# Kernel optimization log

Measured on AMD Instinct MI355X. Metric: run time of the kernel, lower is better.

## Reference

```python
import jax, jax.numpy as jnp
import numpy as np

B, S, D, H = 2, 2048, 1024, 16
HD = D // H  # head dim = 64


def setup_inputs() -> dict:
    key = jax.random.key(0)
    ks = jax.random.split(key, 8)
    s = 0.02
    return {
        "Q": jax.random.normal(ks[0], (B, S, D), jnp.float32),
        "K": jax.random.normal(ks[1], (B, S, D), jnp.float32),
        "V": jax.random.normal(ks[2], (B, S, D), jnp.float32),
        "mask": jax.random.randint(ks[3], (1, 1, S, S), 0, 2, jnp.int32),
        "Wq": jax.random.normal(ks[4], (D, D), jnp.float32) * s,
        "bq": jnp.zeros((D,), jnp.float32),
        "Wk": jax.random.normal(ks[5], (D, D), jnp.float32) * s,
        "bk": jnp.zeros((D,), jnp.float32),
        "Wv": jax.random.normal(ks[6], (D, D), jnp.float32) * s,
        "bv": jnp.zeros((D,), jnp.float32),
        "Wo": jax.random.normal(ks[7], (D, D), jnp.float32) * s,
        "bo": jnp.zeros((D,), jnp.float32),
    }


def reference(Q, K, V, mask, Wq, bq, Wk, bk, Wv, bv, Wo, bo):
    b = Q.shape[0]
    # QKV projections, split into heads: [B,S,D] -> [B,H,S,HD]
    q = (Q @ Wq + bq).reshape(b, -1, H, HD).transpose(0, 2, 1, 3)
    k = (K @ Wk + bk).reshape(b, -1, H, HD).transpose(0, 2, 1, 3)
    v = (V @ Wv + bv).reshape(b, -1, H, HD).transpose(0, 2, 1, 3)
    # scaled dot-product attention with full [B,H,S,S] scores (as in source)
    scale = jnp.sqrt(jnp.asarray(HD, q.dtype))
    scores = jnp.einsum("bhqd,bhkd->bhqk", q, k) / scale
    scores = jnp.where(mask == 0, -jnp.inf, scores)
    attn = jax.nn.softmax(scores, axis=-1)
    ctx = jnp.einsum("bhqk,bhkd->bhqd", attn, v)
    # merge heads and output projection
    concat = ctx.transpose(0, 2, 1, 3).reshape(b, -1, H * HD)
    return concat @ Wo + bo
```

## Files before the change

### kernel.cpp

```cpp
#include <hip/hip_runtime.h>


using s8v = __attribute__((ext_vector_type(8))) short;
using f4v = __attribute__((ext_vector_type(4))) float;
typedef unsigned long long u64;

__device__ __forceinline__ unsigned short f2bf(float f) {
  union { float f; unsigned int u; } v; v.f = f;
  return (unsigned short)((v.u + 0x7fffu + ((v.u >> 16) & 1u)) >> 16);
}

__global__ void f2b3_kernel(const float* __restrict__ A, const float* __restrict__ B,
                            const float* __restrict__ C, unsigned short* __restrict__ oA,
                            unsigned short* __restrict__ oB, unsigned short* __restrict__ oC) {
  int z = blockIdx.x >> 12;
  int idx = (blockIdx.x & 4095) * 256 + threadIdx.x;
  const float* in = (z == 0) ? A : (z == 1) ? B : C;
  unsigned short* out = (z == 0) ? oA : (z == 1) ? oB : oC;
  float4 v = ((const float4*)in)[idx];
  ushort4 o;
  o.x = f2bf(v.x); o.y = f2bf(v.y); o.z = f2bf(v.z); o.w = f2bf(v.w);
  ((ushort4*)out)[idx] = o;
}

__global__ void packmask_kernel(const int* __restrict__ mask, u64* __restrict__ bm) {
  int gw = (int)((blockIdx.x * 256 + threadIdx.x) >> 6);
  int lane = threadIdx.x & 63;
  int mv = mask[(size_t)gw * 64 + lane];
  u64 bal = __ballot(mv != 0);
  if (lane == 0) bm[gw] = bal;
}

__global__ void wtrans4_kernel(const float* __restrict__ W0, const float* __restrict__ W1,
                               const float* __restrict__ W2, const float* __restrict__ W3,
                               unsigned short* __restrict__ T0, unsigned short* __restrict__ T1,
                               unsigned short* __restrict__ T2, unsigned short* __restrict__ T3) {
  __shared__ unsigned short t[64][72];
  int z = blockIdx.z;
  const float* W = (z == 0) ? W0 : (z == 1) ? W1 : (z == 2) ? W2 : W3;
  unsigned short* Wt = (z == 0) ? T0 : (z == 1) ? T1 : (z == 2) ? T2 : T3;
  int k0 = blockIdx.x * 64, n0 = blockIdx.y * 64;
  int tid = threadIdx.x;
  for (int p = 0; p < 4; ++p) {
    int idx = p * 256 + tid;
    int row = idx >> 4;
    int c4  = idx & 15;
    float4 v = *(const float4*)&W[(size_t)(k0 + row) * 1024 + n0 + c4 * 4];
    t[row][c4 * 4 + 0] = f2bf(v.x);
    t[row][c4 * 4 + 1] = f2bf(v.y);
    t[row][c4 * 4 + 2] = f2bf(v.z);
    t[row][c4 * 4 + 3] = f2bf(v.w);
  }
  __syncthreads();
  for (int p = 0; p < 2; ++p) {
    int idx = p * 256 + tid;
    int j  = idx >> 3;
    int c8 = idx & 7;
    unsigned short tmp[8];
    for (int i = 0; i < 8; ++i) tmp[i] = t[c8 * 8 + i][j];
    uint4 o;
    o.x = tmp[0] | ((unsigned)tmp[1] << 16);
    o.y = tmp[2] | ((unsigned)tmp[3] << 16);
    o.z = tmp[4] | ((unsigned)tmp[5] << 16);
    o.w = tmp[6] | ((unsigned)tmp[7] << 16);
    *(uint4*)&Wt[(size_t)(n0 + j) * 1024 + k0 + c8 * 8] = o;
  }
}

__global__ __launch_bounds__(256) void proj3_kernel(
    const unsigned short* __restrict__ A0, const unsigned short* __restrict__ A1,
    const unsigned short* __restrict__ A2,
    const unsigned short* __restrict__ W0, const unsigned short* __restrict__ W1,
    const unsigned short* __restrict__ W2,
    const float* __restrict__ b0, const float* __restrict__ b1, const float* __restrict__ b2,
    unsigned short* __restrict__ oq, unsigned short* __restrict__ ok,
    unsigned short* __restrict__ ovt) {
  const int z = blockIdx.z;
  const unsigned short* A  = (z == 0) ? A0 : (z == 1) ? A1 : A2;
  const unsigned short* Wt = (z == 0) ? W0 : (z == 1) ? W1 : W2;
  const float* bias        = (z == 0) ? b0 : (z == 1) ? b1 : b2;

  __shared__ __align__(16) unsigned short As[128][40];
  __shared__ __align__(16) unsigned short Bs[128][40];

  const int tid = threadIdx.x;
  const int lane = tid & 63, w = tid >> 6, ln = lane & 15, quad = lane >> 4;
  const int wm = (w & 1) * 64, wn = (w >> 1) * 64;
  const int m0 = blockIdx.x * 128, n0 = blockIdx.y * 128;

  const int r0 = tid >> 2, c40 = tid & 3;
  const int r1 = (tid + 256) >> 2, c41 = tid & 3;

  uint4 ar0 = *(const uint4*)&A[(size_t)(m0 + r0) * 1024 + c40 * 8];
  uint4 ar1 = *(const uint4*)&A[(size_t)(m0 + r1) * 1024 + c41 * 8];
  uint4 br0 = *(const uint4*)&Wt[(size_t)(n0 + r0) * 1024 + c40 * 8];
  uint4 br1 = *(const uint4*)&Wt[(size_t)(n0 + r1) * 1024 + c41 * 8];

  f4v zero = {0.f, 0.f, 0.f, 0.f};
  f4v acc[4][4];
  for (int mi = 0; mi < 4; ++mi)
    for (int ni = 0; ni < 4; ++ni) acc[mi][ni] = zero;

  for (int kt = 0; kt < 1024; kt += 32) {
    *(uint4*)&As[r0][c40 * 8] = ar0;
    *(uint4*)&As[r1][c41 * 8] = ar1;
    *(uint4*)&Bs[r0][c40 * 8] = br0;
    *(uint4*)&Bs[r1][c41 * 8] = br1;
    if (kt + 32 < 1024) {
      ar0 = *(const uint4*)&A[(size_t)(m0 + r0) * 1024 + kt + 32 + c40 * 8];
      ar1 = *(const uint4*)&A[(size_t)(m0 + r1) * 1024 + kt + 32 + c41 * 8];
      br0 = *(const uint4*)&Wt[(size_t)(n0 + r0) * 1024 + kt + 32 + c40 * 8];
      br1 = *(const uint4*)&Wt[(size_t)(n0 + r1) * 1024 + kt + 32 + c41 * 8];
    }
    __syncthreads();
    s8v a[4], b[4];
    for (int mi = 0; mi < 4; ++mi) a[mi] = *(const s8v*)&As[wm + mi * 16 + ln][quad * 8];
    for (int ni = 0; ni < 4; ++ni) b[ni] = *(const s8v*)&Bs[wn + ni * 16 + ln][quad * 8];
    for (int mi = 0; mi < 4; ++mi)
      for (int ni = 0; ni < 4; ++ni)
        acc[mi][ni] = __builtin_amdgcn_mfma_f32_16x16x32_bf16(a[mi], b[ni], acc[mi][ni], 0, 0, 0);
    __syncthreads();
  }

  const float qscale = (z == 0) ? 0.18033688f : 1.0f;
  if (z < 2) {
    unsigned short* outp = (z == 0) ? oq : ok;
    for (int mi = 0; mi < 4; ++mi) {
      int rb = m0 + wm + mi * 16 + quad * 4;
      int b_ = rb >> 11;
      for (int ni = 0; ni < 4; ++ni) {
        int col = n0 + wn + ni * 16 + ln;
        float bvv = bias[col];
        int h = col >> 6, hd = col & 63;
        size_t ob = (size_t)(b_ * 16 + h) * 2048;
        for (int r = 0; r < 4; ++r) {
          int s = (rb + r) & 2047;
          outp[(ob + s) * 64 + hd] = f2bf((acc[mi][ni][r] + bvv) * qscale);
        }
      }
    }
  } else {
    for (int mi = 0; mi < 4; ++mi) {
      int rb = m0 + wm + mi * 16 + quad * 4;
      int b_ = rb >> 11, s = rb & 2047;
      for (int ni = 0; ni < 4; ++ni) {
        int col = n0 + wn + ni * 16 + ln;
        float bvv = bias[col];
        int h = col >> 6, hd = col & 63;
        ushort4 o;
        o.x = f2bf(acc[mi][ni][0] + bvv);
        o.y = f2bf(acc[mi][ni][1] + bvv);
        o.z = f2bf(acc[mi][ni][2] + bvv);
        o.w = f2bf(acc[mi][ni][3] + bvv);
        *(ushort4*)&ovt[((size_t)(b_ * 16 + h) * 64 + hd) * 2048 + s] = o;
      }
    }
  }
}

__global__ __launch_bounds__(256) void flash_kernel(
    const unsigned short* __restrict__ q, const unsigned short* __restrict__ k,
    const unsigned short* __restrict__ vt, const u64* __restrict__ bm,
    unsigned short* __restrict__ ctx) {
  __shared__ __align__(16) unsigned short qp_s[64][72];
  __shared__ __align__(16) unsigned short k_s[64][72];
  __shared__ __align__(16) unsigned short v_s[64][72];

  const int tid = threadIdx.x;
  const int lane = tid & 63, w = tid >> 6, ln = lane & 15, quad = lane >> 4;
  const int q0 = blockIdx.x * 64;
  const int bh = blockIdx.y;
  const unsigned short* qg  = q  + ((size_t)bh * 2048 + q0) * 64;
  const unsigned short* kgb = k  + (size_t)bh * 2048 * 64;
  const unsigned short* vgb = vt + (size_t)bh * 64 * 2048;
  const u64* bmr = bm + (size_t)(q0 + w * 16 + quad * 4) * 32;

  for (int p = 0; p < 2; ++p) {
    int c = p * 256 + tid;
    int row = c >> 3, c8 = c & 7;
    *(uint4*)&qp_s[row][c8 * 8] = *(const uint4*)&qg[(size_t)row * 64 + c8 * 8];
  }
  __syncthreads();
  s8v aq[2];
  aq[0] = *(const s8v*)&qp_s[w * 16 + ln][quad * 8];
  aq[1] = *(const s8v*)&qp_s[w * 16 + ln][32 + quad * 8];

  const int srow0 = tid >> 3, sc8 = tid & 7;
  const int srow1 = 32 + srow0;

  uint4 kr0 = *(const uint4*)&kgb[(size_t)srow0 * 64 + sc8 * 8];
  uint4 kr1 = *(const uint4*)&kgb[(size_t)srow1 * 64 + sc8 * 8];
  uint4 vr0 = *(const uint4*)&vgb[(size_t)srow0 * 2048 + sc8 * 8];
  uint4 vr1 = *(const uint4*)&vgb[(size_t)srow1 * 2048 + sc8 * 8];
  u64 mwc[4], mwn[4];
  for (int r = 0; r < 4; ++r) mwc[r] = bmr[r * 32];

  f4v zero = {0.f, 0.f, 0.f, 0.f};
  float lsum[4] = {0.f, 0.f, 0.f, 0.f};
  f4v o_acc[4];
  for (int ni = 0; ni < 4; ++ni) o_acc[ni] = zero;

  for (int kt = 0; kt < 2048; kt += 64) {
    *(uint4*)&k_s[srow0][sc8 * 8] = kr0;
    *(uint4*)&k_s[srow1][sc8 * 8] = kr1;
    *(uint4*)&v_s[srow0][sc8 * 8] = vr0;
    *(uint4*)&v_s[srow1][sc8 * 8] = vr1;
    if (kt + 64 < 2048) {
      int ktn = kt + 64;
      kr0 = *(const uint4*)&kgb[(size_t)(ktn + srow0) * 64 + sc8 * 8];
      kr1 = *(const uint4*)&kgb[(size_t)(ktn + srow1) * 64 + sc8 * 8];
      vr0 = *(const uint4*)&vgb[(size_t)srow0 * 2048 + ktn + sc8 * 8];
      vr1 = *(const uint4*)&vgb[(size_t)srow1 * 2048 + ktn + sc8 * 8];
      int ktcn = ktn >> 6;
      for (int r = 0; r < 4; ++r) mwn[r] = bmr[r * 32 + ktcn];
    }
    __syncthreads();

    f4v sc[4];
    for (int ni = 0; ni < 4; ++ni) {
      sc[ni] = zero;
      s8v bk0 = *(const s8v*)&k_s[ni * 16 + ln][quad * 8];
      s8v bk1 = *(const s8v*)&k_s[ni * 16 + ln][32 + quad * 8];
      sc[ni] = __builtin_amdgcn_mfma_f32_16x16x32_bf16(aq[0], bk0, sc[ni], 0, 0, 0);
      sc[ni] = __builtin_amdgcn_mfma_f32_16x16x32_bf16(aq[1], bk1, sc[ni], 0, 0, 0);
    }

    for (int r = 0; r < 4; ++r) {
      u64 m = mwc[r] >> ln;
      unsigned mlo = (unsigned)m, mhi = (unsigned)(m >> 32);
      float f[4];
      f[0] = (float)(mlo & 1u);
      f[1] = (float)((mlo >> 16) & 1u);
      f[2] = (float)(mhi & 1u);
      f[3] = (float)((mhi >> 16) & 1u);
      for (int ni = 0; ni < 4; ++ni) {
        float e = __builtin_amdgcn_exp2f(sc[ni][r]) * f[ni];
        unsigned int u = __float_as_uint(e);
        lsum[r] += __uint_as_float(u & 0xffff0000u);
        qp_s[w * 16 + quad * 4 + r][ni * 16 + ln] = (unsigned short)(u >> 16);
      }
    }
    for (int r = 0; r < 4; ++r) mwc[r] = mwn[r];

    s8v ap0 = *(const s8v*)&qp_s[w * 16 + ln][quad * 8];
    s8v ap1 = *(const s8v*)&qp_s[w * 16 + ln][32 + quad * 8];
    for (int ni = 0; ni < 4; ++ni) {
      s8v bv0 = *(const s8v*)&v_s[ni * 16 + ln][quad * 8];
      s8v bv1 = *(const s8v*)&v_s[ni * 16 + ln][32 + quad * 8];
      o_acc[ni] = __builtin_amdgcn_mfma_f32_16x16x32_bf16(ap0, bv0, o_acc[ni], 0, 0, 0);
      o_acc[ni] = __builtin_amdgcn_mfma_f32_16x16x32_bf16(ap1, bv1, o_acc[ni], 0, 0, 0);
    }
    __syncthreads();
  }

  int b_ = bh >> 4, h = bh & 15;
  for (int r = 0; r < 4; ++r) {
    float l = lsum[r];
    for (int off = 1; off < 16; off <<= 1) l += __shfl_xor(l, off);
    float inv = 1.f / l;
    int srow = q0 + w * 16 + quad * 4 + r;
    size_t base = ((size_t)b_ * 2048 + srow) * 1024 + h * 64;
    for (int ni = 0; ni < 4; ++ni)
      ctx[base + ni * 16 + ln] = f2bf(o_acc[ni][r] * inv);
  }
}

__global__ __launch_bounds__(256) void gemm_out_kernel(
    const unsigned short* __restrict__ A, const unsigned short* __restrict__ Wt,
    const float* __restrict__ bias, float* __restrict__ out) {
  __shared__ __align__(16) unsigned short As[128][40];
  __shared__ __align__(16) unsigned short Bs[128][40];

  const int tid = threadIdx.x;
  const int lane = tid & 63, w = tid >> 6, ln = lane & 15, quad = lane >> 4;
  const int wm = (w & 1) * 64, wn = (w >> 1) * 64;
  const int m0 = blockIdx.x * 128, n0 = blockIdx.y * 128;

  const int r0 = tid >> 2, c40 = tid & 3;
  const int r1 = (tid + 256) >> 2, c41 = tid & 3;

  uint4 ar0 = *(const uint4*)&A[(size_t)(m0 + r0) * 1024 + c40 * 8];
  uint4 ar1 = *(const uint4*)&A[(size_t)(m0 + r1) * 1024 + c41 * 8];
  uint4 br0 = *(const uint4*)&Wt[(size_t)(n0 + r0) * 1024 + c40 * 8];
  uint4 br1 = *(const uint4*)&Wt[(size_t)(n0 + r1) * 1024 + c41 * 8];

  f4v zero = {0.f, 0.f, 0.f, 0.f};
  f4v acc[4][4];
  for (int mi = 0; mi < 4; ++mi)
    for (int ni = 0; ni < 4; ++ni) acc[mi][ni] = zero;

  for (int kt = 0; kt < 1024; kt += 32) {
    *(uint4*)&As[r0][c40 * 8] = ar0;
    *(uint4*)&As[r1][c41 * 8] = ar1;
    *(uint4*)&Bs[r0][c40 * 8] = br0;
    *(uint4*)&Bs[r1][c41 * 8] = br1;
    if (kt + 32 < 1024) {
      ar0 = *(const uint4*)&A[(size_t)(m0 + r0) * 1024 + kt + 32 + c40 * 8];
      ar1 = *(const uint4*)&A[(size_t)(m0 + r1) * 1024 + kt + 32 + c41 * 8];
      br0 = *(const uint4*)&Wt[(size_t)(n0 + r0) * 1024 + kt + 32 + c40 * 8];
      br1 = *(const uint4*)&Wt[(size_t)(n0 + r1) * 1024 + kt + 32 + c41 * 8];
    }
    __syncthreads();
    s8v a[4], b[4];
    for (int mi = 0; mi < 4; ++mi) a[mi] = *(const s8v*)&As[wm + mi * 16 + ln][quad * 8];
    for (int ni = 0; ni < 4; ++ni) b[ni] = *(const s8v*)&Bs[wn + ni * 16 + ln][quad * 8];
    for (int mi = 0; mi < 4; ++mi)
      for (int ni = 0; ni < 4; ++ni)
        acc[mi][ni] = __builtin_amdgcn_mfma_f32_16x16x32_bf16(a[mi], b[ni], acc[mi][ni], 0, 0, 0);
    __syncthreads();
  }

  for (int mi = 0; mi < 4; ++mi) {
    int rb = m0 + wm + mi * 16 + quad * 4;
    for (int ni = 0; ni < 4; ++ni) {
      int col = n0 + wn + ni * 16 + ln;
      float bvv = bias[col];
      for (int r = 0; r < 4; ++r)
        out[(size_t)(rb + r) * 1024 + col] = acc[mi][ni][r] + bvv;
    }
  }
}

extern "C" void kernel_launch(void* const* d_in, const int* in_sizes, int n_in,
                              void* d_out, int out_size, void* d_ws, size_t ws_size,
                              hipStream_t stream) {
  const float* Q  = (const float*)d_in[0];
  const float* K  = (const float*)d_in[1];
  const float* V  = (const float*)d_in[2];
  const int* mask = (const int*)d_in[3];
  const float* Wq = (const float*)d_in[4];
  const float* bq = (const float*)d_in[5];
  const float* Wk = (const float*)d_in[6];
  const float* bk = (const float*)d_in[7];
  const float* Wv = (const float*)d_in[8];
  const float* bv = (const float*)d_in[9];
  const float* Wo = (const float*)d_in[10];
  const float* bo = (const float*)d_in[11];
  float* out = (float*)d_out;

  char* ws = (char*)d_ws;
  const size_t MB = 1u << 20;
  unsigned short* qb  = (unsigned short*)(ws + 0 * MB);
  unsigned short* kb  = (unsigned short*)(ws + 8 * MB);
  unsigned short* vb  = (unsigned short*)(ws + 16 * MB);
  unsigned short* wqt = (unsigned short*)(ws + 24 * MB);
  unsigned short* wkt = (unsigned short*)(ws + 26 * MB);
  unsigned short* wvt = (unsigned short*)(ws + 28 * MB);
  unsigned short* wot = (unsigned short*)(ws + 30 * MB);
  unsigned short* qh  = (unsigned short*)(ws + 32 * MB);
  unsigned short* kh  = (unsigned short*)(ws + 40 * MB);
  unsigned short* vth = (unsigned short*)(ws + 48 * MB);
  unsigned short* ctx = (unsigned short*)(ws + 56 * MB);
  u64* bm = (u64*)(ws + 0 * MB);

  f2b3_kernel<<<12288, 256, 0, stream>>>(Q, K, V, qb, kb, vb);
  wtrans4_kernel<<<dim3(16, 16, 4), 256, 0, stream>>>(Wq, Wk, Wv, Wo, wqt, wkt, wvt, wot);
  proj3_kernel<<<dim3(32, 8, 3), 256, 0, stream>>>(qb, kb, vb, wqt, wkt, wvt,
                                                   bq, bk, bv, qh, kh, vth);
  packmask_kernel<<<16384, 256, 0, stream>>>(mask, bm);
  flash_kernel<<<dim3(32, 32), 256, 0, stream>>>(qh, kh, vth, bm, ctx);
  gemm_out_kernel<<<dim3(32, 8), 256, 0, stream>>>(ctx, wot, bo, out);
}
```

Before: 276.8 us.

## Process 128 query rows per flash block and transpose score MFMA layout

Each flash-attention block now covers 128 query rows, with every wave handling two 16-row strips. Each K/V tile loaded into shared memory is therefore reused across twice as many queries, which halves K/V global traffic and syncs per query. The QK^T MFMA operands are swapped so that each lane holds four consecutive key columns for one query row. That lets P be written to shared memory as packed 64-bit stores and means one mask word per strip instead of four. The cost is half as many blocks (512), so occupancy is lower, along with higher register pressure from the doubled accumulators.

```diff
diff --git a/kernel.cpp b/kernel.cpp
--- a/kernel.cpp
+++ b/kernel.cpp
@@ -162,43 +162,48 @@
     const unsigned short* __restrict__ q, const unsigned short* __restrict__ k,
     const unsigned short* __restrict__ vt, const u64* __restrict__ bm,
     unsigned short* __restrict__ ctx) {
-  __shared__ __align__(16) unsigned short qp_s[64][72];
+  __shared__ __align__(16) unsigned short qp_s[128][72];
   __shared__ __align__(16) unsigned short k_s[64][72];
   __shared__ __align__(16) unsigned short v_s[64][72];
 
   const int tid = threadIdx.x;
   const int lane = tid & 63, w = tid >> 6, ln = lane & 15, quad = lane >> 4;
-  const int q0 = blockIdx.x * 64;
+  const int q0 = blockIdx.x * 128;
   const int bh = blockIdx.y;
   const unsigned short* qg  = q  + ((size_t)bh * 2048 + q0) * 64;
   const unsigned short* kgb = k  + (size_t)bh * 2048 * 64;
   const unsigned short* vgb = vt + (size_t)bh * 64 * 2048;
-  const u64* bmr = bm + (size_t)(q0 + w * 16 + quad * 4) * 32;
-
-  for (int p = 0; p < 2; ++p) {
+
+  for (int p = 0; p < 4; ++p) {
     int c = p * 256 + tid;
     int row = c >> 3, c8 = c & 7;
     *(uint4*)&qp_s[row][c8 * 8] = *(const uint4*)&qg[(size_t)row * 64 + c8 * 8];
   }
   __syncthreads();
-  s8v aq[2];
-  aq[0] = *(const s8v*)&qp_s[w * 16 + ln][quad * 8];
-  aq[1] = *(const s8v*)&qp_s[w * 16 + ln][32 + quad * 8];
+  s8v aq[2][2];
+  for (int s = 0; s < 2; ++s)
+    for (int h = 0; h < 2; ++h)
+      aq[s][h] = *(const s8v*)&qp_s[s * 64 + w * 16 + ln][h * 32 + quad * 8];
 
   const int srow0 = tid >> 3, sc8 = tid & 7;
   const int srow1 = 32 + srow0;
+
+  const u64* bmr0 = bm + (size_t)(q0 + w * 16 + ln) * 32;
+  const u64* bmr1 = bmr0 + 64 * 32;
 
   uint4 kr0 = *(const uint4*)&kgb[(size_t)srow0 * 64 + sc8 * 8];
   uint4 kr1 = *(const uint4*)&kgb[(size_t)srow1 * 64 + sc8 * 8];
   uint4 vr0 = *(const uint4*)&vgb[(size_t)srow0 * 2048 + sc8 * 8];
   uint4 vr1 = *(const uint4*)&vgb[(size_t)srow1 * 2048 + sc8 * 8];
-  u64 mwc[4], mwn[4];
-  for (int r = 0; r < 4; ++r) mwc[r] = bmr[r * 32];
+  u64 mwc[2], mwn[2];
+  mwc[0] = bmr0[0];
+  mwc[1] = bmr1[0];
 
   f4v zero = {0.f, 0.f, 0.f, 0.f};
-  float lsum[4] = {0.f, 0.f, 0.f, 0.f};
-  f4v o_acc[4];
-  for (int ni = 0; ni < 4; ++ni) o_acc[ni] = zero;
+  float lsum[2] = {0.f, 0.f};
+  f4v o_acc[2][4];
+  for (int s = 0; s < 2; ++s)
+    for (int ni = 0; ni < 4; ++ni) o_acc[s][ni] = zero;
 
   for (int kt = 0; kt < 2048; kt += 64) {
     *(uint4*)&k_s[srow0][sc8 * 8] = kr0;
@@ -212,56 +217,70 @@
       vr0 = *(const uint4*)&vgb[(size_t)srow0 * 2048 + ktn + sc8 * 8];
       vr1 = *(const uint4*)&vgb[(size_t)srow1 * 2048 + ktn + sc8 * 8];
       int ktcn = ktn >> 6;
-      for (int r = 0; r < 4; ++r) mwn[r] = bmr[r * 32 + ktcn];
-    }
-    __syncthreads();
-
-    f4v sc[4];
+      mwn[0] = bmr0[ktcn];
+      mwn[1] = bmr1[ktcn];
+    }
+    __syncthreads();
+
+    f4v sc[2][4];
     for (int ni = 0; ni < 4; ++ni) {
-      sc[ni] = zero;
-      s8v bk0 = *(const s8v*)&k_s[ni * 16 + ln][quad * 8];
-      s8v bk1 = *(const s8v*)&k_s[ni * 16 + ln][32 + quad * 8];
-      sc[ni] = __builtin_amdgcn_mfma_f32_16x16x32_bf16(aq[0], bk0, sc[ni], 0, 0, 0);
-      sc[ni] = __builtin_amdgcn_mfma_f32_16x16x32_bf16(aq[1], bk1, sc[ni], 0, 0, 0);
-    }
-
-    for (int r = 0; r < 4; ++r) {
-      u64 m = mwc[r] >> ln;
+      s8v ak0 = *(const s8v*)&k_s[ni * 16 + ln][quad * 8];
+      s8v ak1 = *(const s8v*)&k_s[ni * 16 + ln][32 + quad * 8];
+      for (int s = 0; s < 2; ++s) {
+        f4v t = zero;
+        t = __builtin_amdgcn_mfma_f32_16x16x32_bf16(ak0, aq[s][0], t, 0, 0, 0);
+        t = __builtin_amdgcn_mfma_f32_16x16x32_bf16(ak1, aq[s][1], t, 0, 0, 0);
+        sc[s][ni] = t;
+      }
+    }
+
+    for (int s = 0; s < 2; ++s) {
+      u64 m = mwc[s] >> (quad * 4);
       unsigned mlo = (unsigned)m, mhi = (unsigned)(m >> 32);
-      float f[4];
-      f[0] = (float)(mlo & 1u);
-      f[1] = (float)((mlo >> 16) & 1u);
-      f[2] = (float)(mhi & 1u);
-      f[3] = (float)((mhi >> 16) & 1u);
+      float lacc = 0.f;
       for (int ni = 0; ni < 4; ++ni) {
-        float e = __builtin_amdgcn_exp2f(sc[ni][r]) * f[ni];
-        unsigned int u = __float_as_uint(e);
-        lsum[r] += __uint_as_float(u & 0xffff0000u);
-        qp_s[w * 16 + quad * 4 + r][ni * 16 + ln] = (unsigned short)(u >> 16);
-      }
-    }
-    for (int r = 0; r < 4; ++r) mwc[r] = mwn[r];
-
-    s8v ap0 = *(const s8v*)&qp_s[w * 16 + ln][quad * 8];
-    s8v ap1 = *(const s8v*)&qp_s[w * 16 + ln][32 + quad * 8];
+        unsigned msel = ((ni < 2) ? mlo : mhi) >> ((ni & 1) * 16);
+        u64 pk = 0;
+        for (int r = 0; r < 4; ++r) {
+          float e = __builtin_amdgcn_exp2f(sc[s][ni][r]) * (float)((msel >> r) & 1u);
+          unsigned u = __float_as_uint(e);
+          lacc += __uint_as_float(u & 0xffff0000u);
+          pk |= (u64)(u >> 16) << (16 * r);
+        }
+        *(u64*)&qp_s[s * 64 + w * 16 + ln][ni * 16 + quad * 4] = pk;
+      }
+      lsum[s] += lacc;
+      mwc[s] = mwn[s];
+    }
+
+    s8v ap[2][2];
+    for (int s = 0; s < 2; ++s)
+      for (int h = 0; h < 2; ++h)
+        ap[s][h] = *(const s8v*)&qp_s[s * 64 + w * 16 + ln][h * 32 + quad * 8];
     for (int ni = 0; ni < 4; ++ni) {
       s8v bv0 = *(const s8v*)&v_s[ni * 16 + ln][quad * 8];
       s8v bv1 = *(const s8v*)&v_s[ni * 16 + ln][32 + quad * 8];
-      o_acc[ni] = __builtin_amdgcn_mfma_f32_16x16x32_bf16(ap0, bv0, o_acc[ni], 0, 0, 0);
-      o_acc[ni] = __builtin_amdgcn_mfma_f32_16x16x32_bf16(ap1, bv1, o_acc[ni], 0, 0, 0);
+      for (int s = 0; s < 2; ++s) {
+        o_acc[s][ni] = __builtin_amdgcn_mfma_f32_16x16x32_bf16(ap[s][0], bv0, o_acc[s][ni], 0, 0, 0);
+        o_acc[s][ni] = __builtin_amdgcn_mfma_f32_16x16x32_bf16(ap[s][1], bv1, o_acc[s][ni], 0, 0, 0);
+      }
     }
     __syncthreads();
   }
 
   int b_ = bh >> 4, h = bh & 15;
-  for (int r = 0; r < 4; ++r) {
-    float l = lsum[r];
-    for (int off = 1; off < 16; off <<= 1) l += __shfl_xor(l, off);
-    float inv = 1.f / l;
-    int srow = q0 + w * 16 + quad * 4 + r;
-    size_t base = ((size_t)b_ * 2048 + srow) * 1024 + h * 64;
-    for (int ni = 0; ni < 4; ++ni)
-      ctx[base + ni * 16 + ln] = f2bf(o_acc[ni][r] * inv);
+  for (int s = 0; s < 2; ++s) {
+    float l = lsum[s];
+    l += __shfl_xor(l, 16);
+    l += __shfl_xor(l, 32);
+    for (int r = 0; r < 4; ++r) {
+      float lr = __shfl(l, quad * 4 + r);
+      float inv = 1.f / lr;
+      int srow = q0 + s * 64 + w * 16 + quad * 4 + r;
+      size_t base = ((size_t)b_ * 2048 + srow) * 1024 + h * 64;
+      for (int ni = 0; ni < 4; ++ni)
+        ctx[base + ni * 16 + ln] = f2bf(o_acc[s][ni][r] * inv);
+    }
   }
 }
 
@@ -358,6 +377,6 @@
   proj3_kernel<<<dim3(32, 8, 3), 256, 0, stream>>>(qb, kb, vb, wqt, wkt, wvt,
                                                    bq, bk, bv, qh, kh, vth);
   packmask_kernel<<<16384, 256, 0, stream>>>(mask, bm);
-  flash_kernel<<<dim3(32, 32), 256, 0, stream>>>(qh, kh, vth, bm, ctx);
+  flash_kernel<<<dim3(16, 32), 256, 0, stream>>>(qh, kh, vth, bm, ctx);
   gemm_out_kernel<<<dim3(32, 8), 256, 0, stream>>>(ctx, wot, bo, out);
 }
```

Measured after the change: 270.8 us. 2.2% less time.
